# Optimization experiments

Measured on AMD Instinct MI355X. Metric: run time of the kernel, lower is better.

The kernel has to match this reference:

```python
import jax, jax.numpy as jnp
import numpy as np

H = 3  # hidden size (matches nn.LSTM(3, 3, ...))


def _lstm_dir(x, Wih, Whh, bih, bhh, reverse):
    """One direction of one LSTM layer. x: [B,T,D]; PyTorch gate order i,f,g,o."""
    B = x.shape[0]
    xT = jnp.swapaxes(x, 0, 1)  # [T,B,D]
    # Precompute input projection for all timesteps (memory-bound GEMM once).
    x_proj = jnp.einsum('tbd,gd->tbg', xT, Wih) + (bih + bhh)  # [T,B,4H]

    def step(carry, xp):
        h, c = carry
        gates = xp + h @ Whh.T  # [B,4H]
        i = jax.nn.sigmoid(gates[:, :H])
        f = jax.nn.sigmoid(gates[:, H:2 * H])
        g = jnp.tanh(gates[:, 2 * H:3 * H])
        o = jax.nn.sigmoid(gates[:, 3 * H:])
        c = f * c + i * g
        h = o * jnp.tanh(c)
        return (h, c), h

    init = (jnp.zeros((B, H), x.dtype), jnp.zeros((B, H), x.dtype))
    _, hs = jax.lax.scan(step, init, x_proj, reverse=reverse)
    return jnp.swapaxes(hs, 0, 1)  # [B,T,H], time-aligned with input


def setup_inputs() -> dict:
    key = jax.random.key(0)
    ks = jax.random.split(key, 20)
    B, T = 8192, 512
    k = 1.0 / np.sqrt(H)

    def u(kk, shape):
        return jax.random.uniform(kk, shape, jnp.float32, -k, k)

    inp = {"x": jax.random.normal(ks[0], (B, T, 3), jnp.float32)}
    # layer 0: input dim 3; layer 1: input dim 2*H = 6
    inp.update({
        "W_ih_l0": u(ks[1], (4 * H, 3)),  "W_hh_l0": u(ks[2], (4 * H, H)),
        "b_ih_l0": u(ks[3], (4 * H,)),    "b_hh_l0": u(ks[4], (4 * H,)),
        "W_ih_l0r": u(ks[5], (4 * H, 3)), "W_hh_l0r": u(ks[6], (4 * H, H)),
        "b_ih_l0r": u(ks[7], (4 * H,)),   "b_hh_l0r": u(ks[8], (4 * H,)),
        "W_ih_l1": u(ks[9], (4 * H, 2 * H)),  "W_hh_l1": u(ks[10], (4 * H, H)),
        "b_ih_l1": u(ks[11], (4 * H,)),       "b_hh_l1": u(ks[12], (4 * H,)),
        "W_ih_l1r": u(ks[13], (4 * H, 2 * H)),"W_hh_l1r": u(ks[14], (4 * H, H)),
        "b_ih_l1r": u(ks[15], (4 * H,)),      "b_hh_l1r": u(ks[16], (4 * H,)),
        "W_lin": u(ks[17], (1, 2 * H)),       "b_lin": u(ks[18], (1,)),
    })
    return inp


def reference(x, W_ih_l0, W_hh_l0, b_ih_l0, b_hh_l0,
              W_ih_l0r, W_hh_l0r, b_ih_l0r, b_hh_l0r,
              W_ih_l1, W_hh_l1, b_ih_l1, b_hh_l1,
              W_ih_l1r, W_hh_l1r, b_ih_l1r, b_hh_l1r,
              W_lin, b_lin):
    # layer 0 (bidirectional)
    y0 = jnp.concatenate([
        _lstm_dir(x, W_ih_l0, W_hh_l0, b_ih_l0, b_hh_l0, False),
        _lstm_dir(x, W_ih_l0r, W_hh_l0r, b_ih_l0r, b_hh_l0r, True),
    ], axis=-1)  # [B,T,6]
    # layer 1 (bidirectional)
    y1 = jnp.concatenate([
        _lstm_dir(y0, W_ih_l1, W_hh_l1, b_ih_l1, b_hh_l1, False),
        _lstm_dir(y0, W_ih_l1r, W_hh_l1r, b_ih_l1r, b_hh_l1r, True),
    ], axis=-1)  # [B,T,6]
    last = y1[:, -1, :]  # [B,6]  (output sequence at final timestep)
    out = last @ W_lin.T + b_lin  # [B,1]
    return jax.nn.sigmoid(out.reshape(-1))  # [B]
```

## Files before the change

### kernel.cpp

```cpp
#include <hip/hip_runtime.h>


#define B_ 8192
#define T_ 512
#define LOG2E 1.4426950408889634f

typedef float v2f __attribute__((ext_vector_type(2)));

__device__ __forceinline__ float rcp_(float x)  { return __builtin_amdgcn_rcpf(x); }
__device__ __forceinline__ float exp2_(float x) { return __builtin_amdgcn_exp2f(x); }
__device__ __forceinline__ float sigm_(float x) {
  return rcp_(1.0f + exp2_(-LOG2E * x));
}
__device__ __forceinline__ float tanh_(float x) {
  return 1.0f - 2.0f * rcp_(1.0f + exp2_(2.0f * LOG2E * x));
}
__device__ __forceinline__ v2f sp(float s) { return (v2f){s, s}; }
__device__ __forceinline__ v2f pkfma(v2f a, float b, v2f c) {
  return __builtin_elementwise_fma(a, sp(b), c);
}

template <int CTRL>
__device__ __forceinline__ float dppf(float v) {
  int s = __float_as_int(v);
  return __int_as_float(__builtin_amdgcn_update_dpp(s, s, CTRL, 0xF, 0xF, false));
}
#define QB0 0x00
#define QB1 0x55
#define QB2 0xAA
#define SHR4 0x114

__device__ __forceinline__ float el(const float4* a, int i) {
  const float4 v = a[i >> 2];
  const int r = i & 3;
  return r == 0 ? v.x : r == 1 ? v.y : r == 2 ? v.z : v.w;
}

__global__ __launch_bounds__(256, 1) void lstm_l0_bwd(
    const float* __restrict__ x,
    const float* __restrict__ Wih, const float* __restrict__ Whh,
    const float* __restrict__ bih, const float* __restrict__ bhh,
    float* __restrict__ y0b)
{
  int tid = blockIdx.x * 256 + threadIdx.x;
  int b = tid >> 2, jl = tid & 3;
  int j = (jl < 3) ? jl : 0;

  v2f wif[6], wgo[6];
#pragma unroll
  for (int k = 0; k < 3; ++k) {
    wif[k]   = (v2f){ Wih[j*3+k],     Wih[(3+j)*3+k] };
    wif[3+k] = (v2f){ Whh[j*3+k],     Whh[(3+j)*3+k] };
    wgo[k]   = (v2f){ Wih[(6+j)*3+k], Wih[(9+j)*3+k] };
    wgo[3+k] = (v2f){ Whh[(6+j)*3+k], Whh[(9+j)*3+k] };
  }
  v2f bif = (v2f){ bih[j]+bhh[j],     bih[3+j]+bhh[3+j] };
  v2f bgo = (v2f){ bih[6+j]+bhh[6+j], bih[9+j]+bhh[9+j] };

  float h = 0.f, c = 0.f, hb0 = 0.f, hb1 = 0.f, hb2 = 0.f;
  const float4* xq = (const float4*)(x + (size_t)b * (T_ * 3));
  float* yw = y0b + (size_t)b * (T_ * 3) + jl;

  float4 A4[6], B4[6];
  auto LD = [&](int blk, float4* dst) {
#pragma unroll
    for (int k = 0; k < 6; ++k) dst[k] = xq[blk * 6 + k];
    __builtin_amdgcn_sched_barrier(0);
  };
  auto STEP = [&](float x0, float x1, float x2, int t) {
    v2f aif = pkfma(wif[0], x0, bif);
    aif = pkfma(wif[1], x1, aif);
    aif = pkfma(wif[2], x2, aif);
    v2f uif = wif[3] * sp(hb0);
    uif = pkfma(wif[4], hb1, uif);
    uif = pkfma(wif[5], hb2, uif);
    v2f pif = aif + uif;
    v2f ago = pkfma(wgo[0], x0, bgo);
    ago = pkfma(wgo[1], x1, ago);
    ago = pkfma(wgo[2], x2, ago);
    v2f ugo = wgo[3] * sp(hb0);
    ugo = pkfma(wgo[4], hb1, ugo);
    ugo = pkfma(wgo[5], hb2, ugo);
    v2f pgo = ago + ugo;

    v2f eif = pif * sp(-LOG2E);
    float ig = rcp_(1.f + exp2_(eif.x));
    float fg = rcp_(1.f + exp2_(eif.y));
    float gg = tanh_(pgo.x);
    float og = sigm_(pgo.y);
    c = fg * c + ig * gg;
    h = og * tanh_(c);
    hb0 = dppf<QB0>(h); hb1 = dppf<QB1>(h); hb2 = dppf<QB2>(h);
    if (jl < 3) yw[(((t + 1) & (T_ - 1))) * 3] = h;
  };
  auto PROC = [&](int blk, const float4* v) {
#pragma unroll
    for (int s = 7; s >= 0; --s) STEP(el(v,s*3), el(v,s*3+1), el(v,s*3+2), blk*8+s);
  };

  LD(63, A4); LD(62, B4);
  for (int blk = 63; blk >= 1; blk -= 2) {
    PROC(blk, A4);
    if (blk >= 3) LD(blk - 2, A4);
    PROC(blk - 1, B4);
    if (blk >= 3) LD(blk - 3, B4);
  }
}

__global__ __launch_bounds__(256, 1) void lstm_fused_fwd(
    const float* __restrict__ x,
    const float* __restrict__ Wih0, const float* __restrict__ Whh0,
    const float* __restrict__ bih0, const float* __restrict__ bhh0,
    const float* __restrict__ Wih1, const float* __restrict__ Whh1,
    const float* __restrict__ bih1, const float* __restrict__ bhh1,
    const float* __restrict__ Wih1r, const float* __restrict__ Whh1r,
    const float* __restrict__ bih1r, const float* __restrict__ bhh1r,
    const float* __restrict__ Wlin, const float* __restrict__ blin,
    const float* __restrict__ y0b,
    float* __restrict__ out)
{
  int tid = blockIdx.x * 256 + threadIdx.x;
  int b = tid >> 3, lane = tid & 7;
  bool role1 = lane >= 4;
  int j  = role1 ? (lane - 4) : lane;
  int jc = (j < 3) ? j : 2;

  v2f wif[9], wgo[9];
  v2f bif, bgo;
  if (!role1) {
#pragma unroll
    for (int k = 0; k < 3; ++k) {
      wif[k]   = (v2f){ Wih0[jc*3+k],     Wih0[(3+jc)*3+k] };
      wgo[k]   = (v2f){ Wih0[(6+jc)*3+k], Wih0[(9+jc)*3+k] };
      wif[3+k] = (v2f){ 0.f, 0.f };
      wgo[3+k] = (v2f){ 0.f, 0.f };
      wif[6+k] = (v2f){ Whh0[jc*3+k],     Whh0[(3+jc)*3+k] };
      wgo[6+k] = (v2f){ Whh0[(6+jc)*3+k], Whh0[(9+jc)*3+k] };
    }
    bif = (v2f){ bih0[jc]+bhh0[jc],     bih0[3+jc]+bhh0[3+jc] };
    bgo = (v2f){ bih0[6+jc]+bhh0[6+jc], bih0[9+jc]+bhh0[9+jc] };
  } else {
#pragma unroll
    for (int k = 0; k < 6; ++k) {
      wif[k] = (v2f){ Wih1[jc*6+k],     Wih1[(3+jc)*6+k] };
      wgo[k] = (v2f){ Wih1[(6+jc)*6+k], Wih1[(9+jc)*6+k] };
    }
#pragma unroll
    for (int k = 0; k < 3; ++k) {
      wif[6+k] = (v2f){ Whh1[jc*3+k],     Whh1[(3+jc)*3+k] };
      wgo[6+k] = (v2f){ Whh1[(6+jc)*3+k], Whh1[(9+jc)*3+k] };
    }
    bif = (v2f){ bih1[jc]+bhh1[jc],     bih1[3+jc]+bhh1[3+jc] };
    bgo = (v2f){ bih1[6+jc]+bhh1[6+jc], bih1[9+jc]+bhh1[9+jc] };
  }

  float h = 0.f, c = 0.f;
  float ha0 = 0.f, ha1 = 0.f, ha2 = 0.f;
  float hb0 = 0.f, hb1 = 0.f, hb2 = 0.f;
  const float4* baseq =
      (const float4*)((role1 ? y0b : x) + (size_t)b * (T_ * 3));

  const float* up = y0b + (size_t)b * (T_ * 3);
  float ub0 = up[0], ub1 = up[1], ub2 = up[2];

  float4 A4[6], B4[6];
  auto LD = [&](int blk, float4* dst) {
#pragma unroll
    for (int k = 0; k < 6; ++k) dst[k] = baseq[blk * 6 + k];
    __builtin_amdgcn_sched_barrier(0);
  };
  auto STEP = [&](float L0, float L1, float L2, bool valid) {
    float v0 = role1 ? hb0 : L0;
    float v1 = role1 ? hb1 : L1;
    float v2 = role1 ? hb2 : L2;
    v2f aif = pkfma(wif[0], v0, bif);
    aif = pkfma(wif[1], v1, aif);
    aif = pkfma(wif[2], v2, aif);
    aif = pkfma(wif[3], L0, aif);
    aif = pkfma(wif[4], L1, aif);
    v2f uif = wif[5] * sp(L2);
    uif = pkfma(wif[6], ha0, uif);
    uif = pkfma(wif[7], ha1, uif);
    uif = pkfma(wif[8], ha2, uif);
    v2f pif = aif + uif;
    v2f ago = pkfma(wgo[0], v0, bgo);
    ago = pkfma(wgo[1], v1, ago);
    ago = pkfma(wgo[2], v2, ago);
    ago = pkfma(wgo[3], L0, ago);
    ago = pkfma(wgo[4], L1, ago);
    v2f ugo = wgo[5] * sp(L2);
    ugo = pkfma(wgo[6], ha0, ugo);
    ugo = pkfma(wgo[7], ha1, ugo);
    ugo = pkfma(wgo[8], ha2, ugo);
    v2f pgo = ago + ugo;

    v2f eif = pif * sp(-LOG2E);
    float ig = rcp_(1.f + exp2_(eif.x));
    float fg = rcp_(1.f + exp2_(eif.y));
    float gg = tanh_(pgo.x);
    float og = sigm_(pgo.y);
    float cn = fg * c + ig * gg;
    float hn = og * tanh_(cn);
    c = valid ? cn : c;
    h = valid ? hn : h;
    ha0 = dppf<QB0>(h); ha1 = dppf<QB1>(h); ha2 = dppf<QB2>(h);
    hb0 = dppf<SHR4>(ha0); hb1 = dppf<SHR4>(ha1); hb2 = dppf<SHR4>(ha2);
  };
  auto PROC = [&](int blk, const float4* v) {
#pragma unroll
    for (int s = 0; s < 8; ++s) {
      int tt = blk * 8 + s;
      bool valid = role1 ? (tt != 0) : true;
      STEP(el(v,s*3), el(v,s*3+1), el(v,s*3+2), valid);
    }
  };

  LD(0, A4); LD(1, B4);
  for (int blk = 0; blk < 64; blk += 2) {
    PROC(blk, A4);
    if (blk + 2 < 64) LD(blk + 2, A4);
    PROC(blk + 1, B4);
    if (blk + 3 < 64) LD(blk + 3, B4);
  }
  STEP(ub0, ub1, ub2, role1);

  float e0 = role1 ? hb0 : ha0;
  float e1 = role1 ? hb1 : ha1;
  float e2 = role1 ? hb2 : ha2;

  float h1b;
  {
    float wr[4][6], br[4];
#pragma unroll
    for (int g = 0; g < 4; ++g) {
      int r = g * 3 + jc;
#pragma unroll
      for (int k = 0; k < 6; ++k) wr[g][k] = Wih1r[r*6+k];
      br[g] = bih1r[r] + bhh1r[r];
    }
    float q[4];
#pragma unroll
    for (int g = 0; g < 4; ++g)
      q[g] = br[g] + wr[g][0]*e0 + wr[g][1]*e1 + wr[g][2]*e2
                   + wr[g][3]*ub0 + wr[g][4]*ub1 + wr[g][5]*ub2;
    float ig = sigm_(q[0]), gg = tanh_(q[2]), og = sigm_(q[3]);
    h1b = og * tanh_(ig * gg);
  }

  float part = 0.f;
  if (role1) { if (j < 3) part = Wlin[j]     * h;   }
  else       { if (j < 3) part = Wlin[3 + j] * h1b; }
  part += __shfl_xor(part, 1, 8);
  part += __shfl_xor(part, 2, 8);
  part += __shfl_xor(part, 4, 8);
  if (lane == 0) out[b] = sigm_(part + blin[0]);
}

extern "C" void kernel_launch(void* const* d_in, const int* in_sizes, int n_in,
                              void* d_out, int out_size, void* d_ws, size_t ws_size,
                              hipStream_t stream) {
  const float* x        = (const float*)d_in[0];
  const float* W_ih_l0  = (const float*)d_in[1];
  const float* W_hh_l0  = (const float*)d_in[2];
  const float* b_ih_l0  = (const float*)d_in[3];
  const float* b_hh_l0  = (const float*)d_in[4];
  const float* W_ih_l0r = (const float*)d_in[5];
  const float* W_hh_l0r = (const float*)d_in[6];
  const float* b_ih_l0r = (const float*)d_in[7];
  const float* b_hh_l0r = (const float*)d_in[8];
  const float* W_ih_l1  = (const float*)d_in[9];
  const float* W_hh_l1  = (const float*)d_in[10];
  const float* b_ih_l1  = (const float*)d_in[11];
  const float* b_hh_l1  = (const float*)d_in[12];
  const float* W_ih_l1r = (const float*)d_in[13];
  const float* W_hh_l1r = (const float*)d_in[14];
  const float* b_ih_l1r = (const float*)d_in[15];
  const float* b_hh_l1r = (const float*)d_in[16];
  const float* W_lin    = (const float*)d_in[17];
  const float* b_lin    = (const float*)d_in[18];

  float* y0b = (float*)d_ws;
  float* out = (float*)d_out;

  lstm_l0_bwd<<<(B_ * 4) / 256, 256, 0, stream>>>(
      x, W_ih_l0r, W_hh_l0r, b_ih_l0r, b_hh_l0r, y0b);

  lstm_fused_fwd<<<(B_ * 8) / 256, 256, 0, stream>>>(
      x, W_ih_l0, W_hh_l0, b_ih_l0, b_hh_l0,
      W_ih_l1, W_hh_l1, b_ih_l1, b_hh_l1,
      W_ih_l1r, W_hh_l1r, b_ih_l1r, b_hh_l1r,
      W_lin, b_lin, y0b, out);
}
```

Baseline: 171.4 us.

## Store reverse-layer outputs as per-block channel-major float4 writes

```diff
diff --git a/kernel.cpp b/kernel.cpp
--- a/kernel.cpp
+++ b/kernel.cpp
@@ -59,7 +59,10 @@
 
   float h = 0.f, c = 0.f, hb0 = 0.f, hb1 = 0.f, hb2 = 0.f;
   const float4* xq = (const float4*)(x + (size_t)b * (T_ * 3));
-  float* yw = y0b + (size_t)b * (T_ * 3) + jl;
+  float* ywb = y0b + (size_t)b * (T_ * 3) + jl * 8;
+
+  float hst[8];
+  float h511 = 0.f;
 
   float4 A4[6], B4[6];
   auto LD = [&](int blk, float4* dst) {
@@ -67,7 +70,7 @@
     for (int k = 0; k < 6; ++k) dst[k] = xq[blk * 6 + k];
     __builtin_amdgcn_sched_barrier(0);
   };
-  auto STEP = [&](float x0, float x1, float x2, int t) {
+  auto STEP = [&](float x0, float x1, float x2, int slot) {
     v2f aif = pkfma(wif[0], x0, bif);
     aif = pkfma(wif[1], x1, aif);
     aif = pkfma(wif[2], x2, aif);
@@ -91,20 +94,34 @@
     c = fg * c + ig * gg;
     h = og * tanh_(c);
     hb0 = dppf<QB0>(h); hb1 = dppf<QB1>(h); hb2 = dppf<QB2>(h);
-    if (jl < 3) yw[(((t + 1) & (T_ - 1))) * 3] = h;
-  };
-  auto PROC = [&](int blk, const float4* v) {
-#pragma unroll
-    for (int s = 7; s >= 0; --s) STEP(el(v,s*3), el(v,s*3+1), el(v,s*3+2), blk*8+s);
+    hst[slot] = h;
+  };
+  auto FLUSH = [&](int yblk) {
+    if (jl < 3) {
+      float4* p = (float4*)(ywb + yblk * 24);
+      p[0] = make_float4(hst[0], hst[1], hst[2], hst[3]);
+      p[1] = make_float4(hst[4], hst[5], hst[6], hst[7]);
+    }
+  };
+  auto PROC = [&](int blk, const float4* v, bool first) {
+    STEP(el(v,21), el(v,22), el(v,23), 0);
+    if (first) h511 = hst[0]; else FLUSH(blk + 1);
+#pragma unroll
+    for (int sx = 6; sx >= 0; --sx)
+      STEP(el(v,sx*3), el(v,sx*3+1), el(v,sx*3+2), sx + 1);
   };
 
   LD(63, A4); LD(62, B4);
-  for (int blk = 63; blk >= 1; blk -= 2) {
-    PROC(blk, A4);
+  PROC(63, A4, true);  LD(61, A4);
+  PROC(62, B4, false); LD(60, B4);
+  for (int blk = 61; blk >= 1; blk -= 2) {
+    PROC(blk, A4, false);
     if (blk >= 3) LD(blk - 2, A4);
-    PROC(blk - 1, B4);
+    PROC(blk - 1, B4, false);
     if (blk >= 3) LD(blk - 3, B4);
   }
+  hst[0] = h511;
+  FLUSH(0);
 }
 
 __global__ __launch_bounds__(256, 1) void lstm_fused_fwd(
@@ -161,7 +178,7 @@
       (const float4*)((role1 ? y0b : x) + (size_t)b * (T_ * 3));
 
   const float* up = y0b + (size_t)b * (T_ * 3);
-  float ub0 = up[0], ub1 = up[1], ub2 = up[2];
+  float ub0 = up[0], ub1 = up[8], ub2 = up[16];
 
   float4 A4[6], B4[6];
   auto LD = [&](int blk, float4* dst) {
@@ -210,8 +227,11 @@
 #pragma unroll
     for (int s = 0; s < 8; ++s) {
       int tt = blk * 8 + s;
+      float L0 = role1 ? el(v, 0*8 + s) : el(v, s*3 + 0);
+      float L1 = role1 ? el(v, 1*8 + s) : el(v, s*3 + 1);
+      float L2 = role1 ? el(v, 2*8 + s) : el(v, s*3 + 2);
       bool valid = role1 ? (tt != 0) : true;
-      STEP(el(v,s*3), el(v,s*3+1), el(v,s*3+2), valid);
+      STEP(L0, L1, L2, valid);
     }
   };
 
```

New measurement: 159.6 us. 1.07x faster.
